# Kernel optimization log

Hardware: AMD Instinct MI355X
Metric: run time of the kernel (lower is better)

Reference implementation:

```python
import jax, jax.numpy as jnp
import numpy as np

NPOINT = 1024   # number of sampled centers
NSAMPLE = 32    # neighbors per center
BN_EPS = 1e-5


def setup_inputs() -> dict:
    key = jax.random.key(0)
    ks = jax.random.split(key, 6)
    B, N, C = 8, 4096, 6
    inp = {
        "xyz": jax.random.normal(ks[0], (B, N, 3), jnp.float32),
        "points": jax.random.normal(ks[1], (B, N, C), jnp.float32),
        "W0": jax.random.normal(ks[2], (64, 9), jnp.float32) * 0.1,
        "g0": jnp.ones((64,), jnp.float32),
        "b0": jnp.zeros((64,), jnp.float32),
        "W1": jax.random.normal(ks[3], (64, 64), jnp.float32) * 0.1,
        "g1": jnp.ones((64,), jnp.float32),
        "b1": jnp.zeros((64,), jnp.float32),
        "W2": jax.random.normal(ks[4], (128, 64), jnp.float32) * 0.1,
        "g2": jnp.ones((128,), jnp.float32),
        "b2": jnp.zeros((128,), jnp.float32),
    }
    return inp


def sample_and_group(xyz, points):
    # xyz: [B,N,3], points: [B,N,C]
    B, N, _ = xyz.shape
    stride = N // NPOINT
    new_xyz = xyz[:, ::stride]                      # [B,S,3] deterministic subsample (FPS surrogate)
    # squared pairwise distances via ||a||^2 + ||b||^2 - 2 a.b  -> [B,S,N]
    d = (jnp.sum(new_xyz * new_xyz, -1)[:, :, None]
         + jnp.sum(xyz * xyz, -1)[:, None, :]
         - 2.0 * jnp.einsum('bsd,bnd->bsn', new_xyz, xyz))
    _, idx = jax.lax.top_k(-d, NSAMPLE)             # [B,S,K] KNN indices
    gather = jax.vmap(lambda arr, i: arr[i])        # per-batch gather: [N,C],[S,K] -> [S,K,C]
    g_xyz = gather(xyz, idx) - new_xyz[:, :, None, :]   # relative coords [B,S,K,3]
    g_pts = gather(points, idx)                     # [B,S,K,C]
    new_points = jnp.concatenate([g_xyz, g_pts], -1)    # [B,S,K,3+C]
    return new_xyz, new_points


def mlp_layer(x, W, g, b):
    # Conv2d(1x1, bias=False) == channel contraction; BN2d with batch stats; ReLU
    x = jnp.einsum('bskc,oc->bsko', x, W)
    m = jnp.mean(x, axis=(0, 1, 2))
    v = jnp.var(x, axis=(0, 1, 2))
    x = (x - m) * jax.lax.rsqrt(v + BN_EPS) * g + b
    return jax.nn.relu(x)


def reference(xyz, points, W0, g0, b0, W1, g1, b1, W2, g2, b2):
    new_xyz, x = sample_and_group(xyz, points)      # x: [B,S,K,9]
    x = mlp_layer(x, W0, g0, b0)
    x = mlp_layer(x, W1, g1, b1)
    x = mlp_layer(x, W2, g2, b2)
    new_points = jnp.max(x, axis=2)                 # max-pool over neighbor dim K -> [B,S,128]
    return new_xyz, new_points
```

## Files before the change

kernel.cpp:

```cpp
#include <hip/hip_runtime.h>
#include <float.h>
#include <stdint.h>

#define TOT   262144
#define NPTS  4096
#define KNN   32
#define BN_EPS 1e-5f
#define CAPV  64
#define TILEP 2048

typedef _Float16 f16;
typedef _Float16 f16x2 __attribute__((ext_vector_type(2)));
typedef _Float16 f16x4 __attribute__((ext_vector_type(4)));
typedef _Float16 f16x8 __attribute__((ext_vector_type(8)));
typedef float    f32x4 __attribute__((ext_vector_type(4)));

__device__ __forceinline__ int mbcnt64(unsigned long long m){
  return __builtin_amdgcn_mbcnt_hi((unsigned)(m>>32),
         __builtin_amdgcn_mbcnt_lo((unsigned)(m & 0xffffffffull), 0));
}
__device__ __forceinline__ unsigned f2ord(float f){
  unsigned u = __float_as_uint(f);
  return u ^ (((unsigned)((int)u >> 31)) | 0x80000000u);
}
__device__ __forceinline__ f16x2 bnrelu2(f16x2 x, f16x2 a, f16x2 c){
  f16x2 r = x*a + c;
  const f16 z = (f16)0.f;
  r[0] = r[0] > z ? r[0] : z;
  r[1] = r[1] > z ? r[1] : z;
  return r;
}
__device__ __forceinline__ void writeElem(int n, int e, float qx, float qy, float qz,
    const float* __restrict__ xb3, const float* __restrict__ fb,
    f16* __restrict__ g16){
  float px = xb3[n*3+0], py = xb3[n*3+1], pz = xb3[n*3+2];
  f16 a[16];
  a[0]=(f16)(px-qx); a[1]=(f16)(py-qy); a[2]=(f16)(pz-qz);
  #pragma unroll
  for (int c6=0;c6<6;c6++) a[3+c6] = (f16)fb[n*6+c6];
  #pragma unroll
  for (int i=9;i<16;i++) a[i]=(f16)0.f;
  f16x8 lo, hi;
  #pragma unroll
  for (int i=0;i<8;i++){ lo[i]=a[i]; hi[i]=a[8+i]; }
  *(f16x8*)(g16 + (size_t)e*16)     = lo;
  *(f16x8*)(g16 + (size_t)e*16 + 8) = hi;
}

__global__ __launch_bounds__(256) void knn_gather(
    const float* __restrict__ xyz, const float* __restrict__ pts,
    f16* __restrict__ g16, float* __restrict__ out_newxyz,
    float* __restrict__ s0m){
  __shared__ float4 tile[TILEP];
  __shared__ unsigned wk[8][CAPV];
  __shared__ unsigned short wi[8][CAPV];
  __shared__ unsigned lcnt[8];
  const int tid = threadIdx.x, lane = tid & 63, wv = tid >> 6;
  const int q0 = blockIdx.x*8 + wv*2;
  const int b  = (blockIdx.x*8) >> 10;
  const float* xb3 = xyz + (size_t)b*NPTS*3;
  float qx[2],qy[2],qz[2],qq[2];
  #pragma unroll
  for (int t=0;t<2;t++){
    int n = ((q0+t) & 1023)*4;
    qx[t]=xb3[n*3+0]; qy[t]=xb3[n*3+1]; qz[t]=xb3[n*3+2];
    qq[t]=qx[t]*qx[t]+qy[t]*qy[t]+qz[t]*qz[t];
  }
  if (tid < 8) lcnt[tid] = 0;
  if (lane == 0){
    #pragma unroll
    for (int t=0;t<2;t++){
      out_newxyz[(q0+t)*3+0]=qx[t]; out_newxyz[(q0+t)*3+1]=qy[t];
      out_newxyz[(q0+t)*3+2]=qz[t];
    }
  }

  float dmin[2] = {FLT_MAX, FLT_MAX};
  #pragma unroll 1
  for (int r=0; r<2; ++r){
    __syncthreads();
    #pragma unroll
    for (int k=0;k<8;k++){
      int p = r*TILEP + k*256 + tid;
      float x = xb3[p*3+0], y = xb3[p*3+1], z = xb3[p*3+2];
      tile[k*256+tid] = make_float4(x,y,z, x*x+y*y+z*z);
    }
    __syncthreads();
    #pragma unroll 4
    for (int i=0;i<32;i++){
      float4 P = tile[i*64+lane];
      #pragma unroll
      for (int t=0;t<2;t++){
        float d = (qq[t]+P.w) - 2.f*(qx[t]*P.x+qy[t]*P.y+qz[t]*P.z);
        dmin[t] = d < dmin[t] ? d : dmin[t];
      }
    }
  }
  float sm[2] = {dmin[0], dmin[1]};
  #pragma unroll
  for (int k=2;k<=64;k<<=1){
    #pragma unroll
    for (int j=k>>1;j>0;j>>=1){
      bool keepmin = (((lane&k)==0) == ((lane&j)==0));
      #pragma unroll
      for (int t=0;t<2;t++){
        float o = __shfl_xor(sm[t], j, 64);
        sm[t] = keepmin ? fminf(sm[t],o) : fmaxf(sm[t],o);
      }
    }
  }
  float Uf[2];
  #pragma unroll
  for (int t=0;t<2;t++) Uf[t] = __shfl(sm[t], 31, 64);

  #pragma unroll 1
  for (int r=0; r<2; ++r){
    __syncthreads();
    #pragma unroll
    for (int k=0;k<8;k++){
      int p = r*TILEP + k*256 + tid;
      float x = xb3[p*3+0], y = xb3[p*3+1], z = xb3[p*3+2];
      tile[k*256+tid] = make_float4(x,y,z, x*x+y*y+z*z);
    }
    __syncthreads();
    #pragma unroll 2
    for (int i=0;i<32;i++){
      float4 P = tile[i*64+lane];
      #pragma unroll
      for (int t=0;t<2;t++){
        float d = (qq[t]+P.w) - 2.f*(qx[t]*P.x+qy[t]*P.y+qz[t]*P.z);
        if (d <= Uf[t]){
          unsigned p2 = atomicAdd(&lcnt[wv*2+t], 1u);
          if (p2 < CAPV){
            wk[wv*2+t][p2] = f2ord(d);
            wi[wv*2+t][p2] = (unsigned short)(r*TILEP + i*64 + lane);
          }
        }
      }
    }
  }
  int cnt[2] = {(int)lcnt[wv*2], (int)lcnt[wv*2+1]};

  unsigned long long v[2];
  #pragma unroll
  for (int t=0;t<2;t++){
    unsigned myk = (lane<cnt[t]) ? wk[wv*2+t][lane] : 0xFFFFFFFFu;
    unsigned myi = (lane<cnt[t]) ? wi[wv*2+t][lane] : 0u;
    v[t] = (((unsigned long long)myk)<<16) | myi;
  }
  #pragma unroll
  for (int k=2;k<=64;k<<=1){
    #pragma unroll
    for (int j=k>>1;j>0;j>>=1){
      bool keepmin = (((lane&k)==0) == ((lane&j)==0));
      #pragma unroll
      for (int t=0;t<2;t++){
        unsigned long long o = __shfl_xor(v[t], j, 64);
        v[t] = keepmin ? (v[t]<o?v[t]:o) : (v[t]>o?v[t]:o);
      }
    }
  }

  const float* fb = pts + (size_t)b*NPTS*6;
  #pragma unroll 1
  for (int t=0;t<2;t++){
    const int ebase = (q0+t)*KNN;
    if (cnt[t] <= CAPV){
      if (lane < KNN){
        int n = (int)(v[t] & 0xffffull);
        writeElem(n, ebase+lane, qx[t],qy[t],qz[t], xb3, fb, g16);
      }
    } else {
      unsigned V=0;
      for (int bit=31; bit>=0; --bit){
        unsigned X = V | (1u<<bit);
        int c=0;
        for (int j=0;j<64;j++){
          int n = j*64+lane;
          float px=xb3[n*3], py=xb3[n*3+1], pz=xb3[n*3+2];
          float d = qq[t] + (px*px+py*py+pz*pz)
                  - 2.f*(qx[t]*px+qy[t]*py+qz[t]*pz);
          c += __popcll(__ballot(f2ord(d) < X));
        }
        if (c < KNN) V = X;
      }
      int cnt2=0;
      for (int pass=0; pass<2; ++pass){
        for (int j=0;j<64;j++){
          int n = j*64+lane;
          float px=xb3[n*3], py=xb3[n*3+1], pz=xb3[n*3+2];
          float d = qq[t] + (px*px+py*py+pz*pz)
                  - 2.f*(qx[t]*px+qy[t]*py+qz[t]*pz);
          unsigned kk = f2ord(d);
          bool sel = pass ? (kk==V) : (kk<V);
          unsigned long long msk = __ballot(sel);
          int pos = cnt2 + mbcnt64(msk);
          if (sel && pos < KNN)
            writeElem(n, ebase+pos, qx[t],qy[t],qz[t], xb3, fb, g16);
          cnt2 += __popcll(msk);
        }
      }
    }
  }

  __syncthreads();
  f16   (*Xs)[16][64]  = (f16(*)[16][64])tile;
  float (*red)[16][16] = (float(*)[16][16])((char*)tile + 16384);
  {
    int e = q0*KNN + lane;
    f16x8 lo = *(const f16x8*)(g16 + (size_t)e*16);
    f16x8 hi = *(const f16x8*)(g16 + (size_t)e*16 + 8);
    #pragma unroll
    for (int c=0;c<8;c++) Xs[wv][c][lane]   = lo[c];
    #pragma unroll
    for (int c=0;c<8;c++) Xs[wv][8+c][lane] = hi[c];
  }
  {
    const int c = lane & 15, qd = lane >> 4;
    f16x8 f0 = *(const f16x8*)(&Xs[wv][c][qd*8]);
    f16x8 f1 = *(const f16x8*)(&Xs[wv][c][32+qd*8]);
    if (c == 9){
      #pragma unroll
      for (int i=0;i<8;i++){ f0[i]=(f16)1.f; f1[i]=(f16)1.f; }
    }
    f32x4 acc = {0.f,0.f,0.f,0.f};
    acc = __builtin_amdgcn_mfma_f32_16x16x32_f16(f0, f0, acc, 0,0,0);
    acc = __builtin_amdgcn_mfma_f32_16x16x32_f16(f1, f1, acc, 0,0,0);
    #pragma unroll
    for (int i=0;i<4;i++) red[wv][qd*4+i][c] = acc[i];
  }
  __syncthreads();
  if (tid < 160){
    int row = tid>>4, col = tid&15;
    float vv = red[0][row][col]+red[1][row][col]+red[2][row][col]+red[3][row][col];
    atomicAdd(&s0m[tid], vv);
  }
}

__global__ void finalize0(const float* __restrict__ s0m,
    const float* __restrict__ W0, const float* __restrict__ g0,
    const float* __restrict__ b0, float* __restrict__ ac0,
    const float* __restrict__ W1, const float* __restrict__ W2,
    f16* __restrict__ W0h, f16* __restrict__ W1h, f16* __restrict__ W2h){
  const int tid = threadIdx.x;
  __shared__ float S[160];
  __shared__ float A0s[64];
  if (tid < 160) S[tid] = s0m[tid];
  __syncthreads();
  if (tid < 64){
    float w[9];
    #pragma unroll
    for (int c=0;c<9;c++) w[c]=W0[tid*9+c];
    const float inv = 1.f/(float)TOT;
    float m=0.f;
    #pragma unroll
    for (int c=0;c<9;c++) m = fmaf(w[c], S[c*16+9], m);
    m *= inv;
    float e2=0.f;
    #pragma unroll
    for (int c1=0;c1<9;c1++){
      float t=0.f;
      #pragma unroll
      for (int c2=0;c2<9;c2++) t = fmaf(w[c2], S[c1*16+c2], t);
      e2 = fmaf(w[c1], t, e2);
    }
    e2 *= inv;
    float var = e2 - m*m;
    float a = g0[tid]*rsqrtf(var + BN_EPS);
    ac0[tid]    = a;
    ac0[64+tid] = fmaf(-m, a, b0[tid]);
    A0s[tid]    = a;
  }
  __syncthreads();
  for (int i=tid; i<2048; i+=256){
    int o = i>>5, c = i&31;
    W0h[i] = (f16)(c<9 ? A0s[o]*W0[o*9+c] : 0.f);
  }
  for (int i=tid; i<4096; i+=256) W1h[i] = (f16)W1[i];
  for (int i=tid; i<8192; i+=256) W2h[i] = (f16)W2[i];
}

__global__ __launch_bounds__(256, 2) void layer1s(
    const f16* __restrict__ g16, const f16* __restrict__ W0h,
    const f16* __restrict__ W1h, const float* __restrict__ ac0,
    float* __restrict__ s1g){
  __shared__ f16 sW0[2048];
  __shared__ f16 sW1[4096];
  __shared__ float ac0c[64];
  __shared__ f16 hb0[4][16][72];
  __shared__ float sred[4][128];
  const int tid = threadIdx.x;
  const int lane = tid & 63, wv = tid >> 6;
  const int e16 = lane & 15, q = lane >> 4;
  *(f16x8*)(&sW0[tid*8]) = *(const f16x8*)(W0h + tid*8);
  *(f16x8*)(&sW1[tid*8])        = *(const f16x8*)(W1h + tid*8);
  *(f16x8*)(&sW1[2048 + tid*8]) = *(const f16x8*)(W1h + 2048 + tid*8);
  if (tid < 64) ac0c[tid] = ac0[64+tid];
  __syncthreads();

  const int base = blockIdx.x*256 + wv*64;
  float ssum[16], ssq[16];
  #pragma unroll
  for (int i=0;i<16;i++){ ssum[i]=0.f; ssq[i]=0.f; }

  #pragma unroll 1
  for (int sub=0; sub<4; ++sub){
    int elem = base + sub*16 + e16;
    f16x8 bg = {};
    if (q < 2) bg = *(const f16x8*)(g16 + (size_t)elem*16 + q*8);
    #pragma unroll
    for (int m=0;m<4;m++){
      f32x4 acc = *(const f32x4*)(&ac0c[m*16 + q*4]);
      f16x8 A0f = *(const f16x8*)(&sW0[(m*16+e16)*32 + q*8]);
      acc = __builtin_amdgcn_mfma_f32_16x16x32_f16(A0f, bg, acc, 0,0,0);
      f16x4 w;
      w[0]=(f16)fmaxf(acc[0],0.f); w[1]=(f16)fmaxf(acc[1],0.f);
      w[2]=(f16)fmaxf(acc[2],0.f); w[3]=(f16)fmaxf(acc[3],0.f);
      *(f16x4*)(&hb0[wv][e16][m*16 + q*4]) = w;
    }
    f32x4 acc2[4];
    #pragma unroll
    for (int m=0;m<4;m++) acc2[m] = (f32x4){0.f,0.f,0.f,0.f};
    #pragma unroll
    for (int s=0;s<2;s++){
      f16x8 bh = *(const f16x8*)(&hb0[wv][e16][s*32 + q*8]);
      #pragma unroll
      for (int m=0;m<4;m++){
        f16x8 A1f = *(const f16x8*)(&sW1[(m*16+e16)*64 + s*32 + q*8]);
        acc2[m] = __builtin_amdgcn_mfma_f32_16x16x32_f16(A1f, bh, acc2[m], 0,0,0);
      }
    }
    #pragma unroll
    for (int m=0;m<4;m++)
      #pragma unroll
      for (int i=0;i<4;i++){
        float x = acc2[m][i];
        ssum[m*4+i] += x;
        ssq[m*4+i]  = fmaf(x, x, ssq[m*4+i]);
      }
  }
  #pragma unroll
  for (int t=0;t<16;t++){
    float a = ssum[t], bq = ssq[t];
    #pragma unroll
    for (int off=1; off<16; off<<=1){
      a  += __shfl_xor(a,  off, 64);
      bq += __shfl_xor(bq, off, 64);
    }
    ssum[t]=a; ssq[t]=bq;
  }
  if (e16==0){
    #pragma unroll
    for (int m=0;m<4;m++)
      #pragma unroll
      for (int i=0;i<4;i++){
        int ch = m*16 + q*4 + i;
        sred[wv][ch]    = ssum[m*4+i];
        sred[wv][64+ch] = ssq[m*4+i];
      }
  }
  __syncthreads();
  if (tid < 128){
    float v = sred[0][tid]+sred[1][tid]+sred[2][tid]+sred[3][tid];
    atomicAdd(&s1g[tid], v);
  }
}

__global__ __launch_bounds__(256, 2) void layer2max(
    const f16* __restrict__ g16, const f16* __restrict__ W0h,
    const f16* __restrict__ W1h, const f16* __restrict__ W2h,
    const float* __restrict__ ac0, const float* __restrict__ s1g,
    const float* __restrict__ g1, const float* __restrict__ b1,
    float* __restrict__ maxbuf, float* __restrict__ s2g){
  __shared__ f16 sW0[2048];
  __shared__ f16 sW1[4096];
  __shared__ float ac0c[64];
  __shared__ f16 ac1s[128];
  __shared__ f16 hb0[4][16][72];
  __shared__ f16 hb1[4][2][16][72];
  float (*redbuf)[256] = (float(*)[256])hb0;
  const int tid = threadIdx.x;
  const int lane = tid & 63, wv = tid >> 6;
  const int e16 = lane & 15, q = lane >> 4;
  *(f16x8*)(&sW0[tid*8]) = *(const f16x8*)(W0h + tid*8);
  *(f16x8*)(&sW1[tid*8])        = *(const f16x8*)(W1h + tid*8);
  *(f16x8*)(&sW1[2048 + tid*8]) = *(const f16x8*)(W1h + 2048 + tid*8);
  if (tid < 64) ac0c[tid] = ac0[64+tid];
  if (tid < 64){
    const float inv = 1.f/(float)TOT;
    float m = s1g[tid]*inv;
    float vv = s1g[64+tid]*inv - m*m;
    float a = g1[tid]*rsqrtf(vv + BN_EPS);
    ac1s[tid]    = (f16)a;
    ac1s[64+tid] = (f16)fmaf(-m, a, b1[tid]);
  }
  __syncthreads();

  f16x8 Bw[8][2];
  #pragma unroll
  for (int nt=0;nt<8;nt++)
    #pragma unroll
    for (int s=0;s<2;s++) Bw[nt][s] = *(const f16x8*)(W2h + (nt*16+e16)*64 + s*32 + q*8);

  float ssum[8], ssq[8];
  #pragma unroll
  for (int i=0;i<8;i++){ ssum[i]=0.f; ssq[i]=0.f; }

  #pragma unroll 1
  for (int qq=0; qq<2; ++qq){
    const int qid = blockIdx.x*8 + wv*2 + qq;
    #pragma unroll 1
    for (int mt=0; mt<2; ++mt){
      int elem = qid*32 + mt*16 + e16;
      f16x8 bg = {};
      if (q < 2) bg = *(const f16x8*)(g16 + (size_t)elem*16 + q*8);
      #pragma unroll
      for (int m=0;m<4;m++){
        f32x4 acc = *(const f32x4*)(&ac0c[m*16 + q*4]);
        f16x8 A0f = *(const f16x8*)(&sW0[(m*16+e16)*32 + q*8]);
        acc = __builtin_amdgcn_mfma_f32_16x16x32_f16(A0f, bg, acc, 0,0,0);
        f16x4 w;
        w[0]=(f16)fmaxf(acc[0],0.f); w[1]=(f16)fmaxf(acc[1],0.f);
        w[2]=(f16)fmaxf(acc[2],0.f); w[3]=(f16)fmaxf(acc[3],0.f);
        *(f16x4*)(&hb0[wv][e16][m*16 + q*4]) = w;
      }
      f32x4 acc2[4];
      #pragma unroll
      for (int m=0;m<4;m++) acc2[m] = (f32x4){0.f,0.f,0.f,0.f};
      #pragma unroll
      for (int s=0;s<2;s++){
        f16x8 bh = *(const f16x8*)(&hb0[wv][e16][s*32 + q*8]);
        #pragma unroll
        for (int m=0;m<4;m++){
          f16x8 A1f = *(const f16x8*)(&sW1[(m*16+e16)*64 + s*32 + q*8]);
          acc2[m] = __builtin_amdgcn_mfma_f32_16x16x32_f16(A1f, bh, acc2[m], 0,0,0);
        }
      }
      #pragma unroll
      for (int m=0;m<4;m++){
        f16x4 a4 = *(const f16x4*)(&ac1s[m*16 + q*4]);
        f16x4 c4 = *(const f16x4*)(&ac1s[64 + m*16 + q*4]);
        f16x2 p0 = bnrelu2((f16x2){(f16)acc2[m][0], (f16)acc2[m][1]},
                           (f16x2){a4[0],a4[1]}, (f16x2){c4[0],c4[1]});
        f16x2 p1 = bnrelu2((f16x2){(f16)acc2[m][2], (f16)acc2[m][3]},
                           (f16x2){a4[2],a4[3]}, (f16x2){c4[2],c4[3]});
        f16x4 w; w[0]=p0[0]; w[1]=p0[1]; w[2]=p1[0]; w[3]=p1[1];
        *(f16x4*)(&hb1[wv][mt][e16][m*16 + q*4]) = w;
      }
    }
    float mx[8];
    #pragma unroll
    for (int g=0; g<2; ++g){
      f32x4 acc3[4][2];
      #pragma unroll
      for (int j=0;j<4;j++){ acc3[j][0]=(f32x4){0,0,0,0}; acc3[j][1]=(f32x4){0,0,0,0}; }
      #pragma unroll
      for (int mt=0; mt<2; ++mt)
        #pragma unroll
        for (int s=0;s<2;s++){
          f16x8 af = *(const f16x8*)(&hb1[wv][mt][e16][s*32 + q*8]);
          #pragma unroll
          for (int j=0;j<4;j++)
            acc3[j][mt] = __builtin_amdgcn_mfma_f32_16x16x32_f16(af, Bw[g*4+j][s], acc3[j][mt], 0,0,0);
        }
      #pragma unroll
      for (int j=0;j<4;j++){
        int nt = g*4 + j;
        f32x4 u = acc3[j][0], vv = acc3[j][1];
        float m1 = fmaxf(fmaxf(u[0],u[1]), fmaxf(u[2],u[3]));
        float m2 = fmaxf(fmaxf(vv[0],vv[1]), fmaxf(vv[2],vv[3]));
        float m = fmaxf(m1, m2);
        ssum[nt] += (u[0]+u[1])+(u[2]+u[3]) + (vv[0]+vv[1])+(vv[2]+vv[3]);
        float sq = 0.f;
        #pragma unroll
        for (int i=0;i<4;i++){ sq = fmaf(u[i],u[i],sq); sq = fmaf(vv[i],vv[i],sq); }
        ssq[nt] += sq;
        m = fmaxf(m, __shfl_xor(m, 16, 64));
        m = fmaxf(m, __shfl_xor(m, 32, 64));
        mx[nt] = m;
      }
    }
    if (lane < 16){
      #pragma unroll
      for (int nt=0;nt<8;nt++) maxbuf[(size_t)qid*128 + nt*16 + lane] = mx[nt];
    }
  }
  #pragma unroll
  for (int nt=0;nt<8;nt++){
    ssum[nt] += __shfl_xor(ssum[nt], 16, 64);
    ssum[nt] += __shfl_xor(ssum[nt], 32, 64);
    ssq[nt]  += __shfl_xor(ssq[nt], 16, 64);
    ssq[nt]  += __shfl_xor(ssq[nt], 32, 64);
  }
  __syncthreads();
  if (q==0){
    #pragma unroll
    for (int nt=0;nt<8;nt++){
      redbuf[wv][nt*16+e16]     = ssum[nt];
      redbuf[wv][128+nt*16+e16] = ssq[nt];
    }
  }
  __syncthreads();
  float v = redbuf[0][tid]+redbuf[1][tid]+redbuf[2][tid]+redbuf[3][tid];
  atomicAdd(&s2g[tid], v);
}

__global__ __launch_bounds__(256) void apply2(
    const float4* __restrict__ maxbuf4, const float* __restrict__ s2g,
    const float* __restrict__ g2, const float* __restrict__ b2,
    float4* __restrict__ outp4){
  __shared__ float a2s[128], c2s[128];
  const int tid = threadIdx.x;
  if (tid < 128){
    const float inv = 1.f/(float)TOT;
    float m = s2g[tid]*inv;
    float v = s2g[128+tid]*inv - m*m;
    float a = g2[tid]*rsqrtf(v + BN_EPS);
    a2s[tid] = a;
    c2s[tid] = fmaf(-m, a, b2[tid]);
  }
  __syncthreads();
  int i = blockIdx.x*256 + tid;
  int c4 = (i & 31)*4;
  float4 m = maxbuf4[i];
  float4 r;
  r.x = fmaxf(fmaf(m.x, a2s[c4+0], c2s[c4+0]), 0.f);
  r.y = fmaxf(fmaf(m.y, a2s[c4+1], c2s[c4+1]), 0.f);
  r.z = fmaxf(fmaf(m.z, a2s[c4+2], c2s[c4+2]), 0.f);
  r.w = fmaxf(fmaf(m.w, a2s[c4+3], c2s[c4+3]), 0.f);
  outp4[i] = r;
}

extern "C" void kernel_launch(void* const* d_in, const int* in_sizes, int n_in,
                              void* d_out, int out_size, void* d_ws, size_t ws_size,
                              hipStream_t stream){
  const float* xyz = (const float*)d_in[0];
  const float* pts = (const float*)d_in[1];
  const float* W0  = (const float*)d_in[2];
  const float* g0  = (const float*)d_in[3];
  const float* b0  = (const float*)d_in[4];
  const float* W1  = (const float*)d_in[5];
  const float* g1  = (const float*)d_in[6];
  const float* b1  = (const float*)d_in[7];
  const float* W2  = (const float*)d_in[8];
  const float* g2  = (const float*)d_in[9];
  const float* b2  = (const float*)d_in[10];
  float* out = (float*)d_out;

  float* ws      = (float*)d_ws;
  f16*   g16     = (f16*)ws;
  float* maxbuf  = ws + (size_t)8*TOT;
  float* basep   = ws + (size_t)12*TOT;
  f16*   W0h     = (f16*)basep;
  f16*   W1h     = (f16*)(basep + 1024);
  f16*   W2h     = (f16*)(basep + 3072);
  float* s0m     = basep + 7168;
  float* s1g     = s0m + 160;
  float* s2g     = s1g + 128;
  float* ac0     = s2g + 256;

  (void)hipMemsetAsync(s0m, 0, 544*sizeof(float), stream);
  knn_gather<<<1024, 256, 0, stream>>>(xyz, pts, g16, out, s0m);
  finalize0 <<<   1, 256, 0, stream>>>(s0m, W0, g0, b0, ac0, W1, W2, W0h, W1h, W2h);
  layer1s   <<<1024, 256, 0, stream>>>(g16, W0h, W1h, ac0, s1g);
  layer2max <<<1024, 256, 0, stream>>>(g16, W0h, W1h, W2h, ac0, s1g, g1, b1, maxbuf, s2g);
  apply2    <<<1024, 256, 0, stream>>>((const float4*)maxbuf, s2g, g2, b2, (float4*)(out + 24576));
}
```

Measured before the change: 202.4 us.

## Cache first-pass distances as fp16 in registers instead of recomputing in second pass

The first distance pass now stores each lane's 64 distances per query as packed fp16 in registers. The second pass, which used to reload tiles from global memory into LDS and recompute all distances, now compares the cached fp16 values against a slightly widened threshold. Only candidates that pass are recomputed exactly in fp32 from global memory. This removes a full tile reload, two barriers and most of the recompute, at the cost of 64 extra VGPRs per thread and a risk of lower occupancy. If many near-ties fall inside the widened threshold, the candidate buffer could overflow.

New measurement: 215.5 us. 6.5% more time.

```diff
diff --git a/kernel.cpp b/kernel.cpp
--- a/kernel.cpp
+++ b/kernel.cpp
@@ -76,7 +76,8 @@
   }
 
   float dmin[2] = {FLT_MAX, FLT_MAX};
-  #pragma unroll 1
+  f16x2 dreg[64];
+  #pragma unroll
   for (int r=0; r<2; ++r){
     __syncthreads();
     #pragma unroll
@@ -86,14 +87,17 @@
       tile[k*256+tid] = make_float4(x,y,z, x*x+y*y+z*z);
     }
     __syncthreads();
-    #pragma unroll 4
+    #pragma unroll
     for (int i=0;i<32;i++){
       float4 P = tile[i*64+lane];
+      f16x2 dh;
       #pragma unroll
       for (int t=0;t<2;t++){
         float d = (qq[t]+P.w) - 2.f*(qx[t]*P.x+qy[t]*P.y+qz[t]*P.z);
         dmin[t] = d < dmin[t] ? d : dmin[t];
-      }
+        dh[t] = (f16)d;
+      }
+      dreg[r*32+i] = dh;
     }
   }
   float sm[2] = {dmin[0], dmin[1]};
@@ -109,33 +113,30 @@
       }
     }
   }
-  float Uf[2];
-  #pragma unroll
-  for (int t=0;t<2;t++) Uf[t] = __shfl(sm[t], 31, 64);
-
-  #pragma unroll 1
-  for (int r=0; r<2; ++r){
-    __syncthreads();
-    #pragma unroll
-    for (int k=0;k<8;k++){
-      int p = r*TILEP + k*256 + tid;
-      float x = xb3[p*3+0], y = xb3[p*3+1], z = xb3[p*3+2];
-      tile[k*256+tid] = make_float4(x,y,z, x*x+y*y+z*z);
-    }
-    __syncthreads();
-    #pragma unroll 2
-    for (int i=0;i<32;i++){
-      float4 P = tile[i*64+lane];
-      #pragma unroll
-      for (int t=0;t<2;t++){
-        float d = (qq[t]+P.w) - 2.f*(qx[t]*P.x+qy[t]*P.y+qz[t]*P.z);
-        if (d <= Uf[t]){
-          unsigned p2 = atomicAdd(&lcnt[wv*2+t], 1u);
-          if (p2 < CAPV){
-            wk[wv*2+t][p2] = f2ord(d);
-            wi[wv*2+t][p2] = (unsigned short)(r*TILEP + i*64 + lane);
-          }
-        }
+  f16 uh[2];
+  #pragma unroll
+  for (int t=0;t<2;t++){
+    float Uf = __shfl(sm[t], 31, 64);
+    uh[t] = (f16)(Uf + fmaxf(fabsf(Uf)*0.001953125f, 1e-6f));
+  }
+
+  #pragma unroll
+  for (int i=0;i<64;i++){
+    f16x2 dh = dreg[i];
+    bool h0 = dh[0] <= uh[0], h1 = dh[1] <= uh[1];
+    if (h0 || h1){
+      int n = (i>>5)*TILEP + (i&31)*64 + lane;
+      float px = xb3[n*3+0], py = xb3[n*3+1], pz = xb3[n*3+2];
+      float pw = px*px+py*py+pz*pz;
+      if (h0){
+        float d = (qq[0]+pw) - 2.f*(qx[0]*px+qy[0]*py+qz[0]*pz);
+        unsigned p2 = atomicAdd(&lcnt[wv*2+0], 1u);
+        if (p2 < CAPV){ wk[wv*2+0][p2]=f2ord(d); wi[wv*2+0][p2]=(unsigned short)n; }
+      }
+      if (h1){
+        float d = (qq[1]+pw) - 2.f*(qx[1]*px+qy[1]*py+qz[1]*pz);
+        unsigned p2 = atomicAdd(&lcnt[wv*2+1], 1u);
+        if (p2 < CAPV){ wk[wv*2+1][p2]=f2ord(d); wi[wv*2+1][p2]=(unsigned short)n; }
       }
     }
   }
```
